# Performance work log

Hardware: AMD Instinct MI355X
Metric: run time of the kernel (lower is better)

Reference implementation:

```python
import jax, jax.numpy as jnp
import numpy as np

EPS = 1e-5
S = 4        # s_scale
K = 3        # adjacency subsets
CB = 32      # per-branch channels


def _bn(x, g, b, m, v):
    # inference-mode BatchNorm2d over channel axis 1 of [n,c,t,v]
    scale = g * jax.lax.rsqrt(v + EPS)
    shift = b - m * scale
    return x * scale[None, :, None, None] + shift[None, :, None, None]


def _conv1x1(x, w, b):
    # pointwise conv: x [n,c,t,v], w [o,c], b [o]
    return jnp.einsum('nctv,oc->notv', x, w) + b[None, :, None, None]


def setup_inputs() -> dict:
    key = jax.random.key(0)
    ks = jax.random.split(key, 24)
    d = {}
    d['x'] = jax.random.normal(ks[0], (64, 256, 64, 25), jnp.float32)
    d['A'] = jax.random.uniform(ks[1], (K, 25, 25), jnp.float32)
    d['reduct_w'] = jax.random.normal(ks[2], (128, 256), jnp.float32) * 0.05
    d['reduct_b'] = jax.random.normal(ks[3], (128,), jnp.float32) * 0.05
    d['rg'] = jax.random.uniform(ks[4], (128,), jnp.float32) + 0.5
    d['rb'] = jax.random.normal(ks[5], (128,), jnp.float32) * 0.05
    d['rm'] = jax.random.normal(ks[6], (128,), jnp.float32) * 0.05
    d['rv'] = jax.random.uniform(ks[7], (128,), jnp.float32) + 0.5
    d['gcn_w'] = jax.random.normal(ks[8], (S, K * CB, CB), jnp.float32) * 0.1
    d['gcn_b'] = jax.random.normal(ks[9], (S, K * CB), jnp.float32) * 0.05
    d['PA'] = jax.random.normal(ks[10], (S, K, 25, 25), jnp.float32) * 0.05
    d['bg'] = jax.random.uniform(ks[11], (S, CB), jnp.float32) + 0.5
    d['bb'] = jax.random.normal(ks[12], (S, CB), jnp.float32) * 0.05
    d['bm'] = jax.random.normal(ks[13], (S, CB), jnp.float32) * 0.05
    d['bv'] = jax.random.uniform(ks[14], (S, CB), jnp.float32) + 0.5
    d['exp_w'] = jax.random.normal(ks[15], (256, 128), jnp.float32) * 0.05
    d['exp_b'] = jax.random.normal(ks[16], (256,), jnp.float32) * 0.05
    d['eg'] = jax.random.uniform(ks[17], (256,), jnp.float32) + 0.5
    d['eb'] = jax.random.normal(ks[18], (256,), jnp.float32) * 0.05
    d['em'] = jax.random.normal(ks[19], (256,), jnp.float32) * 0.05
    d['ev'] = jax.random.uniform(ks[20], (256,), jnp.float32) + 0.5
    return d


def reference(x, A, reduct_w, reduct_b, rg, rb, rm, rv, gcn_w, gcn_b, PA,
              bg, bb, bm, bv, exp_w, exp_b, eg, eb, em, ev):
    res = x  # identity residual (in_channels == out_channels)
    h = jax.nn.relu(_bn(_conv1x1(x, reduct_w, reduct_b), rg, rb, rm, rv))
    n, c, t, v = h.shape
    spx = jnp.split(h, S, axis=1)  # S chunks of CB channels
    outs = []
    sp = None
    for i in range(S):  # res2net sequential accumulation ('basic' mode)
        sp = spx[i] if i == 0 else sp + spx[i]
        g = _conv1x1(sp, gcn_w[i], gcn_b[i])           # [n, K*CB, t, v]
        g = g.reshape(n, K, CB, t, v)
        g = jnp.einsum('nkctv,kvw->nctw', g, A + PA[i])
        sp = jax.nn.relu(_bn(g, bg[i], bb[i], bm[i], bv[i]))
        outs.append(sp)
    h = jnp.concatenate(outs, axis=1)                  # [n, 4*CB, t, v]
    out = jax.nn.relu(_bn(_conv1x1(h, exp_w, exp_b), eg, eb, em, ev) + res)
    return out
```

## Files before the change

kernel.cpp:

```cpp
#include <hip/hip_runtime.h>
#include <cstdint>
#include <cstddef>

#define EPSV 1e-5f

using f32x4  = __attribute__((ext_vector_type(4))) float;
using bf16x8 = __attribute__((ext_vector_type(8))) short;

static __device__ __forceinline__ unsigned pk2(float lo, float hi) {
    unsigned a = __builtin_bit_cast(unsigned, lo);
    unsigned b = __builtin_bit_cast(unsigned, hi);
    a = (a + 0x7FFFu + ((a >> 16) & 1u)) >> 16;
    b = (b + 0x7FFFu + ((b >> 16) & 1u)) & 0xFFFF0000u;
    return a | b;
}
static __device__ __forceinline__ unsigned short bf16of(float v) {
    return (unsigned short)(pk2(v, 0.f) & 0xFFFFu);
}
static __device__ __forceinline__ float f32of(unsigned short u) {
    return __builtin_bit_cast(float, (unsigned)u << 16);
}
static __device__ __forceinline__ void unpk2(unsigned u, float& lo, float& hi) {
    lo = __builtin_bit_cast(float, u << 16);
    hi = __builtin_bit_cast(float, u & 0xFFFF0000u);
}

__global__ __launch_bounds__(256) void prep_params(
    const float* __restrict__ rwb, const float* __restrict__ rg,
    const float* __restrict__ rb,  const float* __restrict__ rm,
    const float* __restrict__ rv,
    const float* __restrict__ ewb, const float* __restrict__ eg,
    const float* __restrict__ eb,  const float* __restrict__ em,
    const float* __restrict__ ev,
    const float* __restrict__ bg,  const float* __restrict__ bb,
    const float* __restrict__ bm,  const float* __restrict__ bv,
    float* __restrict__ prm)
{
    int t = threadIdx.x;
    if (t < 128) {
        float sc = rg[t] * rsqrtf(rv[t] + EPSV);
        prm[t]       = sc;
        prm[128 + t] = rb[t] - rm[t] * sc + rwb[t] * sc;
        float bsc = bg[t] * rsqrtf(bv[t] + EPSV);
        prm[768 + t] = bsc;
        prm[896 + t] = bb[t] - bm[t] * bsc;
    }
    {
        float sc = eg[t] * rsqrtf(ev[t] + EPSV);
        prm[256 + t] = sc;
        prm[512 + t] = eb[t] - em[t] * sc + ewb[t] * sc;
    }
}

template<int BMODE, int OUTMODE>
__global__ __launch_bounds__(256) void gemm_v2(
    const void* __restrict__ Bsrc,
    const float* __restrict__ Wt,
    const float* __restrict__ scale,
    const float* __restrict__ shift,
    const float* __restrict__ resid,
    void* __restrict__ OutP,
    int Cin, int O, int P)
{
    const int n    = blockIdx.z;
    const int p0   = blockIdx.x * 64;
    const int o0   = blockIdx.y * 128;
    const int tid  = threadIdx.x;
    const int lane = tid & 63;
    const int wid  = tid >> 6;
    const int wm   = wid >> 1, wn = wid & 1;
    const int rl   = lane & 15;

    __shared__ __align__(16) char smem[32768];
    short* sA = (short*)smem;

    f32x4 acc[4][2];
    #pragma unroll
    for (int i = 0; i < 4; ++i)
        #pragma unroll
        for (int j = 0; j < 2; ++j) acc[i][j] = (f32x4)0.f;

    for (int kc = 0; kc < Cin; kc += 64) {
        if (kc) __syncthreads();

        #pragma unroll
        for (int it = 0; it < 4; ++it) {
            int idx = tid + it * 256;
            int row = idx >> 3, k8 = (idx & 7) << 3;
            const float* wp = Wt + (size_t)(o0 + row) * Cin + kc + k8;
            float4 u = *(const float4*)wp;
            float4 v = *(const float4*)(wp + 4);
            uint4 w = make_uint4(pk2(u.x, u.y), pk2(u.z, u.w),
                                 pk2(v.x, v.y), pk2(v.z, v.w));
            *(uint4*)(&sA[(row << 6) + (k8 ^ ((row & 7) << 3))]) = w;
        }
        if constexpr (BMODE == 0) {
            float* sBf = (float*)(smem + 16384);
            #pragma unroll
            for (int it = 0; it < 4; ++it) {
                int idx = tid + it * 256;
                int k = idx >> 4, p4 = (idx & 15) << 2;
                float4 u = *(const float4*)((const float*)Bsrc
                    + (size_t)n * Cin * P + (size_t)(kc + k) * P + p0 + p4);
                *(float4*)(&sBf[(k << 6) + ((p4 + (((k >> 3) & 7) << 3)) & 63)]) = u;
            }
        } else {
            short* sB = (short*)(smem + 16384);
            #pragma unroll
            for (int it = 0; it < 2; ++it) {
                int idx = tid + it * 256;
                int p = idx >> 3, k8 = (idx & 7) << 3;
                uint4 w = *(const uint4*)((const unsigned short*)Bsrc
                    + ((size_t)n * P + p0 + p) * Cin + kc + k8);
                *(uint4*)(&sB[(p << 6) + (k8 ^ ((p & 7) << 3))]) = w;
            }
        }
        __syncthreads();

        #pragma unroll
        for (int ks = 0; ks < 2; ++ks) {
            const int k0 = ks * 32 + (lane >> 4) * 8;
            bf16x8 af[4], bfr[2];
            #pragma unroll
            for (int i = 0; i < 4; ++i) {
                int row = wm * 64 + i * 16 + rl;
                af[i] = *(const bf16x8*)(&sA[(row << 6) + (k0 ^ ((rl & 7) << 3))]);
            }
            if constexpr (BMODE == 0) {
                const float* sBf = (const float*)(smem + 16384);
                #pragma unroll
                for (int j = 0; j < 2; ++j) {
                    int p = wn * 32 + j * 16 + rl;
                    int base = (p + ((k0 >> 3) << 3)) & 63;
                    float f[8];
                    #pragma unroll
                    for (int q = 0; q < 8; ++q)
                        f[q] = sBf[((k0 + q) << 6) + base];
                    uint4 u = make_uint4(pk2(f[0], f[1]), pk2(f[2], f[3]),
                                         pk2(f[4], f[5]), pk2(f[6], f[7]));
                    bfr[j] = __builtin_bit_cast(bf16x8, u);
                }
            } else {
                const short* sB = (const short*)(smem + 16384);
                #pragma unroll
                for (int j = 0; j < 2; ++j) {
                    int p = wn * 32 + j * 16 + rl;
                    bfr[j] = *(const bf16x8*)(&sB[(p << 6) + (k0 ^ ((rl & 7) << 3))]);
                }
            }
            #pragma unroll
            for (int i = 0; i < 4; ++i)
                #pragma unroll
                for (int j = 0; j < 2; ++j)
                    acc[i][j] = __builtin_amdgcn_mfma_f32_16x16x32_bf16(
                        af[i], bfr[j], acc[i][j], 0, 0, 0);
        }
    }

    if constexpr (OUTMODE == 1) {
        __syncthreads();
        unsigned short* eL = (unsigned short*)smem;
        #pragma unroll
        for (int i = 0; i < 4; ++i) {
            #pragma unroll
            for (int r = 0; r < 4; ++r) {
                int ol = wm * 64 + i * 16 + (lane >> 4) * 4 + r;
                int o  = o0 + ol;
                float sc = scale[o], sh = shift[o];
                #pragma unroll
                for (int j = 0; j < 2; ++j) {
                    int p = wn * 32 + j * 16 + rl;
                    float v = fmaxf(fmaf(acc[i][j][r], sc, sh), 0.f);
                    eL[p * 128 + (ol ^ ((p & 15) << 3))] = bf16of(v);
                }
            }
        }
        __syncthreads();
        unsigned short* out = (unsigned short*)OutP;
        #pragma unroll
        for (int it = 0; it < 4; ++it) {
            int idx = tid + it * 256;
            int p = idx >> 4, m = idx & 15;
            uint4 u = *(const uint4*)(&eL[p * 128 + ((m ^ (p & 15)) << 3)]);
            *(uint4*)(out + ((size_t)n * P + p0 + p) * O + (m << 3)) = u;
        }
    } else {
        __syncthreads();
        float* eT = (float*)smem;
        #pragma unroll
        for (int i = 0; i < 4; ++i) {
            #pragma unroll
            for (int r = 0; r < 4; ++r) {
                int ol = wm * 64 + i * 16 + (lane >> 4) * 4 + r;
                int o  = o0 + ol;
                float sc = scale[o], sh = shift[o];
                #pragma unroll
                for (int j = 0; j < 2; ++j) {
                    int p = wn * 32 + j * 16 + rl;
                    eT[(ol << 6) + ((p + ((ol & 7) << 3)) & 63)] =
                        fmaf(acc[i][j][r], sc, sh);
                }
            }
        }
        __syncthreads();
        float* out = (float*)OutP;
        #pragma unroll
        for (int it = 0; it < 8; ++it) {
            int idx = tid + it * 256;
            int ol = idx >> 4, p4 = (idx & 15) << 2;
            float4 v = *(const float4*)(&eT[(ol << 6) + ((p4 + ((ol & 7) << 3)) & 63)]);
            size_t base = ((size_t)n * O + o0 + ol) * P + p0 + p4;
            if (resid) {
                float4 r4 = *(const float4*)(resid + base);
                v.x += r4.x; v.y += r4.y; v.z += r4.z; v.w += r4.w;
            }
            v.x = fmaxf(v.x, 0.f); v.y = fmaxf(v.y, 0.f);
            v.z = fmaxf(v.z, 0.f); v.w = fmaxf(v.w, 0.f);
            *(float4*)(out + base) = v;
        }
    }
}

__global__ __launch_bounds__(256) void gcn_fused(
    const unsigned short* __restrict__ hT,
    unsigned short* __restrict__ outsT,
    const float* __restrict__ gw,
    const float* __restrict__ gb,
    const float* __restrict__ Aadj,
    const float* __restrict__ PA,
    const float* __restrict__ bsc4,
    const float* __restrict__ bsh4)
{
    const int n  = blockIdx.y;
    const int tt = blockIdx.x;
    const int tid = threadIdx.x;
    const int c  = tid & 31;
    const int tl = tid >> 5;

    __shared__ unsigned short spb[200 * 32];
    __shared__ float wsg[96 * 33];
    __shared__ float Mm[3][25][28];
    __shared__ unsigned short outb[200 * 32];

    const size_t rowbase = (size_t)n * 1600 + (size_t)tt * 200;

    {
        const unsigned short* hrow = hT + rowbase * 128;
        for (int idx = tid; idx < 800; idx += 256) {
            int p = idx >> 2, c8 = (idx & 3) << 3;
            *(uint4*)(&spb[p * 32 + c8]) =
                *(const uint4*)(hrow + (size_t)p * 128 + c8);
        }
        for (int idx = tid; idx < 96 * 32; idx += 256)
            wsg[(idx >> 5) * 33 + (idx & 31)] = gw[idx];
        for (int idx = tid; idx < 1875; idx += 256) {
            int k = idx / 625, rem = idx % 625;
            Mm[k][rem / 25][rem % 25] = Aadj[idx] + PA[idx];
        }
    }
    __syncthreads();

    for (int step = 0; step < 4; ++step) {
        float g[3][25];
        {
            const float* gbp = gb + step * 96;
            float b0 = gbp[c], b1 = gbp[32 + c], b2 = gbp[64 + c];
            #pragma unroll
            for (int v = 0; v < 25; ++v) { g[0][v] = b0; g[1][v] = b1; g[2][v] = b2; }
        }
        const unsigned short* srow = spb + tl * 25 * 32;
        for (int cin = 0; cin < 32; ++cin) {
            float w0 = wsg[c * 33 + cin];
            float w1 = wsg[(32 + c) * 33 + cin];
            float w2 = wsg[(64 + c) * 33 + cin];
            #pragma unroll
            for (int v = 0; v < 25; ++v) {
                float sv = f32of(srow[v * 32 + cin]);
                g[0][v] = fmaf(w0, sv, g[0][v]);
                g[1][v] = fmaf(w1, sv, g[1][v]);
                g[2][v] = fmaf(w2, sv, g[2][v]);
            }
        }

        float out[25];
        #pragma unroll
        for (int w = 0; w < 25; ++w) out[w] = 0.f;
        #pragma unroll
        for (int k = 0; k < 3; ++k)
            #pragma unroll
            for (int v = 0; v < 25; ++v) {
                float gv = g[k][v];
                #pragma unroll
                for (int w = 0; w < 25; ++w)
                    out[w] = fmaf(gv, Mm[k][v][w], out[w]);
            }

        {
            float sc = bsc4[step * 32 + c], sh = bsh4[step * 32 + c];
            #pragma unroll
            for (int w = 0; w < 25; ++w)
                out[w] = fmaxf(fmaf(out[w], sc, sh), 0.f);
        }

        __syncthreads();

        #pragma unroll
        for (int w = 0; w < 25; ++w) {
            unsigned short b = bf16of(out[w]);
            spb[(tl * 25 + w) * 32 + c]  = b;
            outb[(tl * 25 + w) * 32 + c] = b;
        }
        __syncthreads();

        {
            unsigned short* orow = outsT + rowbase * 128 + step * 32;
            for (int idx = tid; idx < 800; idx += 256) {
                int p = idx >> 2, c8 = (idx & 3) << 3;
                uint4 u = *(const uint4*)(&outb[p * 32 + c8]);
                *(uint4*)(orow + (size_t)p * 128 + c8) = u;
            }
        }

        if (step < 3) {
            const unsigned short* hrow = hT + rowbase * 128 + (step + 1) * 32;
            for (int idx = tid; idx < 800; idx += 256) {
                int p = idx >> 2, c8 = (idx & 3) << 3;
                uint4 u = *(const uint4*)(hrow + (size_t)p * 128 + c8);
                uint4 s = *(const uint4*)(&spb[p * 32 + c8]);
                float hf[8], sf[8];
                unpk2(u.x, hf[0], hf[1]); unpk2(u.y, hf[2], hf[3]);
                unpk2(u.z, hf[4], hf[5]); unpk2(u.w, hf[6], hf[7]);
                unpk2(s.x, sf[0], sf[1]); unpk2(s.y, sf[2], sf[3]);
                unpk2(s.z, sf[4], sf[5]); unpk2(s.w, sf[6], sf[7]);
                uint4 r = make_uint4(pk2(sf[0] + hf[0], sf[1] + hf[1]),
                                     pk2(sf[2] + hf[2], sf[3] + hf[3]),
                                     pk2(sf[4] + hf[4], sf[5] + hf[5]),
                                     pk2(sf[6] + hf[6], sf[7] + hf[7]));
                *(uint4*)(&spb[p * 32 + c8]) = r;
            }
            const float* gwp = gw + (step + 1) * 96 * 32;
            for (int idx = tid; idx < 96 * 32; idx += 256)
                wsg[(idx >> 5) * 33 + (idx & 31)] = gwp[idx];
            const float* pap = PA + (step + 1) * 1875;
            for (int idx = tid; idx < 1875; idx += 256) {
                int k = idx / 625, rem = idx % 625;
                Mm[k][rem / 25][rem % 25] = Aadj[idx] + pap[idx];
            }
            __syncthreads();
        }
    }
}

extern "C" void kernel_launch(void* const* d_in, const int* in_sizes, int n_in,
                              void* d_out, int out_size, void* d_ws, size_t ws_size,
                              hipStream_t stream)
{
    const float* x   = (const float*)d_in[0];
    const float* A   = (const float*)d_in[1];
    const float* rw  = (const float*)d_in[2];
    const float* rwb = (const float*)d_in[3];
    const float* rg  = (const float*)d_in[4];
    const float* rb  = (const float*)d_in[5];
    const float* rm  = (const float*)d_in[6];
    const float* rv  = (const float*)d_in[7];
    const float* gw  = (const float*)d_in[8];
    const float* gb  = (const float*)d_in[9];
    const float* PA  = (const float*)d_in[10];
    const float* bg  = (const float*)d_in[11];
    const float* bb  = (const float*)d_in[12];
    const float* bm  = (const float*)d_in[13];
    const float* bv  = (const float*)d_in[14];
    const float* ew  = (const float*)d_in[15];
    const float* ewb = (const float*)d_in[16];
    const float* eg  = (const float*)d_in[17];
    const float* eb  = (const float*)d_in[18];
    const float* em  = (const float*)d_in[19];
    const float* ev  = (const float*)d_in[20];

    char* wsb = (char*)d_ws;
    unsigned short* hT    = (unsigned short*)wsb;
    unsigned short* outsT = (unsigned short*)(wsb + 26214400);
    float*          prm   = (float*)(wsb + 52428800);

    prep_params<<<1, 256, 0, stream>>>(rwb, rg, rb, rm, rv,
                                       ewb, eg, eb, em, ev,
                                       bg, bb, bm, bv, prm);

    gemm_v2<0, 1><<<dim3(25, 1, 64), 256, 0, stream>>>(
        x, rw, prm, prm + 128, nullptr, hT, 256, 128, 1600);

    gcn_fused<<<dim3(8, 64), 256, 0, stream>>>(
        hT, outsT, gw, gb, A, PA, prm + 768, prm + 896);

    gemm_v2<1, 0><<<dim3(25, 2, 64), 256, 0, stream>>>(
        outsT, ew, prm + 256, prm + 512, x, d_out, 128, 256, 1600);
}
```

Baseline: 195.5 us.

## Double-buffer GEMM LDS tiles with register prefetch and padded rows

Rewrites the pointwise-conv GEMM main loop to use a K-tile of 32 with two LDS buffers. The next tile is loaded from global memory into registers while the current tile is computed, which cuts the barriers per tile from two to one. The XOR-swizzled A/B layouts become padded rows (stride 40 bf16). The intent is to hide global load latency behind MFMA work. In exchange it uses more LDS and registers, which may lower occupancy, and the padded layout may bring some bank conflicts.

```diff
diff --git a/kernel.cpp b/kernel.cpp
--- a/kernel.cpp
+++ b/kernel.cpp
@@ -52,8 +52,10 @@
     }
 }
 
+#define LDR 40
+
 template<int BMODE, int OUTMODE>
-__global__ __launch_bounds__(256) void gemm_v2(
+__global__ __launch_bounds__(256) void gemm_v3(
     const void* __restrict__ Bsrc,
     const float* __restrict__ Wt,
     const float* __restrict__ scale,
@@ -71,8 +73,14 @@
     const int wm   = wid >> 1, wn = wid & 1;
     const int rl   = lane & 15;
 
-    __shared__ __align__(16) char smem[32768];
+    constexpr int SMEM = (BMODE == 0)
+        ? (20480 + 16384)
+        : ((20480 + 10240) < 32768 ? 32768 : (20480 + 10240));
+    __shared__ __align__(16) char smem[SMEM];
     short* sA = (short*)smem;
+
+    const int ao = tid >> 1;
+    const int ak = (tid & 1) * 16;
 
     f32x4 acc[4][2];
     #pragma unroll
@@ -80,81 +88,94 @@
         #pragma unroll
         for (int j = 0; j < 2; ++j) acc[i][j] = (f32x4)0.f;
 
-    for (int kc = 0; kc < Cin; kc += 64) {
-        if (kc) __syncthreads();
-
-        #pragma unroll
-        for (int it = 0; it < 4; ++it) {
-            int idx = tid + it * 256;
-            int row = idx >> 3, k8 = (idx & 7) << 3;
-            const float* wp = Wt + (size_t)(o0 + row) * Cin + kc + k8;
-            float4 u = *(const float4*)wp;
-            float4 v = *(const float4*)(wp + 4);
-            uint4 w = make_uint4(pk2(u.x, u.y), pk2(u.z, u.w),
-                                 pk2(v.x, v.y), pk2(v.z, v.w));
-            *(uint4*)(&sA[(row << 6) + (k8 ^ ((row & 7) << 3))]) = w;
-        }
+    float4 ra[4];
+    float4 rb0, rb1;
+    uint4  rbu;
+
+    const int nt = Cin >> 5;
+
+    auto load_regs = [&](int t) {
+        const int kc = t << 5;
+        const float* wrow = Wt + (size_t)(o0 + ao) * Cin + kc + ak;
+        #pragma unroll
+        for (int i = 0; i < 4; ++i)
+            ra[i] = *(const float4*)(wrow + i * 4);
         if constexpr (BMODE == 0) {
-            float* sBf = (float*)(smem + 16384);
-            #pragma unroll
-            for (int it = 0; it < 4; ++it) {
-                int idx = tid + it * 256;
-                int k = idx >> 4, p4 = (idx & 15) << 2;
-                float4 u = *(const float4*)((const float*)Bsrc
-                    + (size_t)n * Cin * P + (size_t)(kc + k) * P + p0 + p4);
-                *(float4*)(&sBf[(k << 6) + ((p4 + (((k >> 3) & 7) << 3)) & 63)]) = u;
-            }
+            const float* bp = (const float*)Bsrc + (size_t)n * Cin * P;
+            int s0 = tid, s1 = tid + 256;
+            rb0 = *(const float4*)(bp + (size_t)(kc + (s0 >> 4)) * P + p0 + ((s0 & 15) << 2));
+            rb1 = *(const float4*)(bp + (size_t)(kc + (s1 >> 4)) * P + p0 + ((s1 & 15) << 2));
         } else {
-            short* sB = (short*)(smem + 16384);
-            #pragma unroll
-            for (int it = 0; it < 2; ++it) {
-                int idx = tid + it * 256;
-                int p = idx >> 3, k8 = (idx & 7) << 3;
-                uint4 w = *(const uint4*)((const unsigned short*)Bsrc
-                    + ((size_t)n * P + p0 + p) * Cin + kc + k8);
-                *(uint4*)(&sB[(p << 6) + (k8 ^ ((p & 7) << 3))]) = w;
-            }
-        }
-        __syncthreads();
-
-        #pragma unroll
-        for (int ks = 0; ks < 2; ++ks) {
-            const int k0 = ks * 32 + (lane >> 4) * 8;
-            bf16x8 af[4], bfr[2];
-            #pragma unroll
-            for (int i = 0; i < 4; ++i) {
-                int row = wm * 64 + i * 16 + rl;
-                af[i] = *(const bf16x8*)(&sA[(row << 6) + (k0 ^ ((rl & 7) << 3))]);
-            }
-            if constexpr (BMODE == 0) {
-                const float* sBf = (const float*)(smem + 16384);
+            const unsigned short* bp = (const unsigned short*)Bsrc;
+            int p = tid >> 2, k8 = (tid & 3) << 3;
+            rbu = *(const uint4*)(bp + ((size_t)n * P + p0 + p) * Cin + kc + k8);
+        }
+    };
+
+    auto write_lds = [&](int buf) {
+        short* a = sA + buf * (128 * LDR);
+        uint4 w0 = make_uint4(pk2(ra[0].x, ra[0].y), pk2(ra[0].z, ra[0].w),
+                              pk2(ra[1].x, ra[1].y), pk2(ra[1].z, ra[1].w));
+        uint4 w1 = make_uint4(pk2(ra[2].x, ra[2].y), pk2(ra[2].z, ra[2].w),
+                              pk2(ra[3].x, ra[3].y), pk2(ra[3].z, ra[3].w));
+        *(uint4*)(a + ao * LDR + ak)     = w0;
+        *(uint4*)(a + ao * LDR + ak + 8) = w1;
+        if constexpr (BMODE == 0) {
+            float* sBf = (float*)(smem + 20480) + buf * 2048;
+            int s0 = tid, s1 = tid + 256;
+            int k0r = s0 >> 4, p40 = (s0 & 15) << 2;
+            int k1r = s1 >> 4, p41 = (s1 & 15) << 2;
+            *(float4*)(&sBf[(k0r << 6) + ((p40 + (((k0r >> 3) & 7) << 3)) & 63)]) = rb0;
+            *(float4*)(&sBf[(k1r << 6) + ((p41 + (((k1r >> 3) & 7) << 3)) & 63)]) = rb1;
+        } else {
+            short* sB = (short*)(smem + 20480) + buf * (64 * LDR);
+            int p = tid >> 2, k8 = (tid & 3) << 3;
+            *(uint4*)(sB + p * LDR + k8) = rbu;
+        }
+    };
+
+    auto compute = [&](int buf) {
+        const short* a = sA + buf * (128 * LDR);
+        const int k0 = (lane >> 4) * 8;
+        bf16x8 af[4], bfr[2];
+        #pragma unroll
+        for (int i = 0; i < 4; ++i)
+            af[i] = *(const bf16x8*)(a + (wm * 64 + i * 16 + rl) * LDR + k0);
+        if constexpr (BMODE == 0) {
+            const float* sBf = (const float*)(smem + 20480) + buf * 2048;
+            #pragma unroll
+            for (int j = 0; j < 2; ++j) {
+                int p = wn * 32 + j * 16 + rl;
+                int base = (p + ((k0 >> 3) << 3)) & 63;
+                float f[8];
                 #pragma unroll
-                for (int j = 0; j < 2; ++j) {
-                    int p = wn * 32 + j * 16 + rl;
-                    int base = (p + ((k0 >> 3) << 3)) & 63;
-                    float f[8];
-                    #pragma unroll
-                    for (int q = 0; q < 8; ++q)
-                        f[q] = sBf[((k0 + q) << 6) + base];
-                    uint4 u = make_uint4(pk2(f[0], f[1]), pk2(f[2], f[3]),
-                                         pk2(f[4], f[5]), pk2(f[6], f[7]));
-                    bfr[j] = __builtin_bit_cast(bf16x8, u);
-                }
-            } else {
-                const short* sB = (const short*)(smem + 16384);
-                #pragma unroll
-                for (int j = 0; j < 2; ++j) {
-                    int p = wn * 32 + j * 16 + rl;
-                    bfr[j] = *(const bf16x8*)(&sB[(p << 6) + (k0 ^ ((rl & 7) << 3))]);
-                }
-            }
-            #pragma unroll
-            for (int i = 0; i < 4; ++i)
-                #pragma unroll
-                for (int j = 0; j < 2; ++j)
-                    acc[i][j] = __builtin_amdgcn_mfma_f32_16x16x32_bf16(
-                        af[i], bfr[j], acc[i][j], 0, 0, 0);
-        }
+                for (int q = 0; q < 8; ++q)
+                    f[q] = sBf[((k0 + q) << 6) + base];
+                uint4 u = make_uint4(pk2(f[0], f[1]), pk2(f[2], f[3]),
+                                     pk2(f[4], f[5]), pk2(f[6], f[7]));
+                bfr[j] = __builtin_bit_cast(bf16x8, u);
+            }
+        } else {
+            const short* sB = (const short*)(smem + 20480) + buf * (64 * LDR);
+            #pragma unroll
+            for (int j = 0; j < 2; ++j)
+                bfr[j] = *(const bf16x8*)(sB + (wn * 32 + j * 16 + rl) * LDR + k0);
+        }
+        #pragma unroll
+        for (int i = 0; i < 4; ++i)
+            #pragma unroll
+            for (int j = 0; j < 2; ++j)
+                acc[i][j] = __builtin_amdgcn_mfma_f32_16x16x32_bf16(
+                    af[i], bfr[j], acc[i][j], 0, 0, 0);
+    };
+
+    load_regs(0);
+    write_lds(0);
+    for (int t = 0; t < nt; ++t) {
+        if (t + 1 < nt) load_regs(t + 1);
+        __syncthreads();
+        compute(t & 1);
+        if (t + 1 < nt) write_lds((t + 1) & 1);
     }
 
     if constexpr (OUTMODE == 1) {
@@ -386,12 +407,12 @@
                                        ewb, eg, eb, em, ev,
                                        bg, bb, bm, bv, prm);
 
-    gemm_v2<0, 1><<<dim3(25, 1, 64), 256, 0, stream>>>(
+    gemm_v3<0, 1><<<dim3(25, 1, 64), 256, 0, stream>>>(
         x, rw, prm, prm + 128, nullptr, hT, 256, 128, 1600);
 
     gcn_fused<<<dim3(8, 64), 256, 0, stream>>>(
         hT, outsT, gw, gb, A, PA, prm + 768, prm + 896);
 
-    gemm_v2<1, 0><<<dim3(25, 2, 64), 256, 0, stream>>>(
+    gemm_v3<1, 0><<<dim3(25, 2, 64), 256, 0, stream>>>(
         outsT, ew, prm + 256, prm + 512, x, d_out, 128, 256, 1600);
 }
```

Result: no change. 194.6 us (-0.5%).
